# Kernel optimization log

Measured on AMD Instinct MI355X. Metric: run time of the kernel, lower is better.

Reference implementation:

```python
import jax, jax.numpy as jnp
from jax import lax
import numpy as np

H_FEAT = 14
W_FEAT = 14
BN_EPS = 1e-5
NORM_EPS = 1e-12

def _coord_tensor():
    # Python-2 integer division as in the original repo
    c = np.zeros((H_FEAT * W_FEAT, 2), dtype=np.float32)
    for i in range(H_FEAT * W_FEAT):
        c[i, 0] = (i // W_FEAT - H_FEAT // 2) / (H_FEAT / 2.0)
        c[i, 1] = (i % W_FEAT - W_FEAT // 2) / (W_FEAT / 2.0)
    return jnp.asarray(c.reshape(1, H_FEAT, W_FEAT, 2).transpose(0, 3, 1, 2))  # [1,2,14,14]

def _l2norm(x, axis):
    n = jnp.linalg.norm(x, axis=axis, keepdims=True)
    return x / jnp.maximum(n, NORM_EPS)

def _conv2d(x, w, b, pad):
    y = lax.conv_general_dilated(x, w, (1, 1), [(pad, pad), (pad, pad)],
                                 dimension_numbers=("NCHW", "OIHW", "NCHW"))
    return y + b[None, :, None, None]

def _bn_train(x, g, b):
    m = x.mean(axis=(0, 2, 3), keepdims=True)
    v = x.var(axis=(0, 2, 3), keepdims=True)
    return (x - m) * lax.rsqrt(v + BN_EPS) * g[None, :, None, None] + b[None, :, None, None]

def _lstm_scan(emb, Wih, Whh, bih, bhh):
    # emb: [T, B, 300]; PyTorch gate order i,f,g,o
    Hdim = Whh.shape[1]
    B = emb.shape[1]
    def step(carry, x):
        h, c = carry
        gates = x @ Wih.T + h @ Whh.T + bih + bhh  # [B, 4H]
        i, f, g, o = jnp.split(gates, 4, axis=-1)
        c = jax.nn.sigmoid(f) * c + jax.nn.sigmoid(i) * jnp.tanh(g)
        h = jax.nn.sigmoid(o) * jnp.tanh(c)
        return (h, c), h
    init = (jnp.zeros((B, Hdim), emb.dtype), jnp.zeros((B, Hdim), emb.dtype))
    _, hs = lax.scan(step, init, emb)
    return hs  # [T, B, H]

def _resblock(v, coord, c1w, c1b, c2w, c2b, bng, bnb):
    B = v.shape[0]
    vin = jnp.concatenate([v, jnp.broadcast_to(coord, (B, 2, H_FEAT, W_FEAT))], axis=1)
    v1 = jax.nn.relu(_conv2d(vin, c1w, c1b, 0))
    v2 = jax.nn.relu(_bn_train(_conv2d(v1, c2w, c2b, 1), bng, bnb))
    return v2 + v1

def setup_inputs() -> dict:
    key = jax.random.key(0)
    ks = jax.random.split(key, 24)
    B, T, V, E = 128, 45, 10000, 300
    Hh = 1024
    s = 0.02
    inp = {}
    inp["que"] = jax.random.randint(ks[0], (B, T), 0, V, dtype=jnp.int64)
    inp["img"] = jax.random.normal(ks[1], (B, 1024, H_FEAT, W_FEAT), dtype=jnp.float32)
    inp["lookup"] = s * jax.random.normal(ks[2], (V + 1, E), dtype=jnp.float32)
    inp["Wih_f"] = s * jax.random.normal(ks[3], (4 * Hh, E), dtype=jnp.float32)
    inp["Whh_f"] = s * jax.random.normal(ks[4], (4 * Hh, Hh), dtype=jnp.float32)
    inp["bih_f"] = jnp.zeros((4 * Hh,), jnp.float32)
    inp["bhh_f"] = jnp.zeros((4 * Hh,), jnp.float32)
    inp["Wih_b"] = s * jax.random.normal(ks[5], (4 * Hh, E), dtype=jnp.float32)
    inp["Whh_b"] = s * jax.random.normal(ks[6], (4 * Hh, Hh), dtype=jnp.float32)
    inp["bih_b"] = jnp.zeros((4 * Hh,), jnp.float32)
    inp["bhh_b"] = jnp.zeros((4 * Hh,), jnp.float32)
    inp["conv0_w"] = s * jax.random.normal(ks[7], (128, 1026, 3, 3), dtype=jnp.float32)
    inp["conv0_b"] = jnp.zeros((128,), jnp.float32)
    inp["bn0_g"] = jnp.ones((128,), jnp.float32)
    inp["bn0_b"] = jnp.zeros((128,), jnp.float32)
    inp["r1c1_w"] = s * jax.random.normal(ks[8], (128, 130, 1, 1), dtype=jnp.float32)
    inp["r1c1_b"] = jnp.zeros((128,), jnp.float32)
    inp["r1c2_w"] = s * jax.random.normal(ks[9], (128, 128, 3, 3), dtype=jnp.float32)
    inp["r1c2_b"] = jnp.zeros((128,), jnp.float32)
    inp["r1bn_g"] = jnp.ones((128,), jnp.float32)
    inp["r1bn_b"] = jnp.zeros((128,), jnp.float32)
    inp["r2c1_w"] = s * jax.random.normal(ks[10], (128, 130, 1, 1), dtype=jnp.float32)
    inp["r2c1_b"] = jnp.zeros((128,), jnp.float32)
    inp["r2c2_w"] = s * jax.random.normal(ks[11], (128, 128, 3, 3), dtype=jnp.float32)
    inp["r2c2_b"] = jnp.zeros((128,), jnp.float32)
    inp["r2bn_g"] = jnp.ones((128,), jnp.float32)
    inp["r2bn_b"] = jnp.zeros((128,), jnp.float32)
    return inp

def reference(que, img, lookup, Wih_f, Whh_f, bih_f, bhh_f, Wih_b, Whh_b, bih_b, bhh_b,
              conv0_w, conv0_b, bn0_g, bn0_b,
              r1c1_w, r1c1_b, r1c2_w, r1c2_b, r1bn_g, r1bn_b,
              r2c1_w, r2c1_b, r2c2_w, r2c2_b, r2bn_g, r2bn_b):
    coord = _coord_tensor()
    # ---- encoder (LSTM mode) ----
    emb = lookup[que]                      # [B, T, 300]
    emb = jnp.transpose(emb, (1, 0, 2))    # [T, B, 300]
    h_f = _lstm_scan(emb, Wih_f, Whh_f, bih_f, bhh_f)
    h_b = _lstm_scan(emb[::-1], Wih_b, Whh_b, bih_b, bhh_b)[::-1]
    qenc = _l2norm(jnp.concatenate([h_f, h_b], axis=-1), axis=-1)  # [T, B, 2048]
    enc = qenc[-1]                                                  # [B, 2048]
    # ---- image branch ----
    v = _l2norm(img, axis=1)               # per-pixel L2 norm over 1024 channels
    B = v.shape[0]
    v = jnp.concatenate([v, jnp.broadcast_to(coord, (B, 2, H_FEAT, W_FEAT))], axis=1)
    v = jax.nn.relu(_bn_train(_conv2d(v, conv0_w, conv0_b, 1), bn0_g, bn0_b))
    v = _resblock(v, coord, r1c1_w, r1c1_b, r1c2_w, r1c2_b, r1bn_g, r1bn_b)
    v = _resblock(v, coord, r2c1_w, r2c1_b, r2c2_w, r2c2_b, r2bn_g, r2bn_b)
    return (enc, v)
```

## Files before the change

### kernel.cpp

```cpp
#include <hip/hip_runtime.h>
#include <math.h>

#define BB   128
#define T    45
#define E    300
#define HH   1024
#define G4   4096
#define HW   196
#define NPX  (BB*HW)
#define C0   1026
#define CM   128
#define CR   130
#define TCH  15

static __device__ __forceinline__ float sigm(float x) { return 1.f / (1.f + __expf(-x)); }

__global__ void k_embed(const int* __restrict__ que, const float* __restrict__ lookup,
                        float* __restrict__ emb) {
    int idx = blockIdx.x * 256 + threadIdx.x;
    if (idx >= T * BB * E) return;
    int e = idx % E;
    int n = idx / E;
    int b = n % BB;
    int t = n / BB;
    int q = que[b * T + t];
    emb[idx] = lookup[(size_t)q * E + e];
}

template <int BM, int BN, int TM, int TN>
__global__ __launch_bounds__(256) void k_gemm_nt(
    const float* __restrict__ A, int lda,
    const float* __restrict__ Bw, int ldb,
    const float* __restrict__ add,
    const float* __restrict__ bias,
    float* __restrict__ C, int ldc,
    int M, int N, int K, int relu) {
    constexpr int KT = 16;
    constexpr int TX = BN / TN;
    __shared__ float As[KT][BM + 4];
    __shared__ float Bs[KT][BN + 4];
    const int tid = threadIdx.x;
    const int tx = tid % TX, ty = tid / TX;
    const int r0 = blockIdx.x * BM, c0 = blockIdx.y * BN;
    float acc[TM][TN] = {};
    for (int k0 = 0; k0 < K; k0 += KT) {
#pragma unroll
        for (int l = tid; l < BM * KT; l += 256) {
            int m = l / KT, k = l % KT;
            int gm = r0 + m, gk = k0 + k;
            As[k][m] = (gm < M && gk < K) ? A[(size_t)gm * lda + gk] : 0.f;
        }
#pragma unroll
        for (int l = tid; l < BN * KT; l += 256) {
            int n = l / KT, k = l % KT;
            int gn = c0 + n, gk = k0 + k;
            Bs[k][n] = (gn < N && gk < K) ? Bw[(size_t)gn * ldb + gk] : 0.f;
        }
        __syncthreads();
#pragma unroll
        for (int k = 0; k < KT; ++k) {
            float ar[TM], br[TN];
#pragma unroll
            for (int i = 0; i < TM; ++i) ar[i] = As[k][ty * TM + i];
#pragma unroll
            for (int j = 0; j < TN; ++j) br[j] = Bs[k][tx * TN + j];
#pragma unroll
            for (int i = 0; i < TM; ++i)
#pragma unroll
                for (int j = 0; j < TN; ++j) acc[i][j] += ar[i] * br[j];
        }
        __syncthreads();
    }
#pragma unroll
    for (int i = 0; i < TM; ++i) {
        int gm = r0 + ty * TM + i;
        if (gm >= M) continue;
#pragma unroll
        for (int j = 0; j < TN; ++j) {
            int gn = c0 + tx * TN + j;
            if (gn >= N) continue;
            float v = acc[i][j];
            if (add) v += add[(size_t)gm * ldc + gn];
            if (bias) v += bias[gn];
            if (relu) v = fmaxf(v, 0.f);
            C[(size_t)gm * ldc + gn] = v;
        }
    }
}

__global__ void k_pack_wih(const float* __restrict__ Wih, float* __restrict__ o) {
    int idx = blockIdx.x * 256 + threadIdx.x;
    if (idx >= G4 * E) return;
    int k = idx % E;
    int n = idx / E;
    o[idx] = Wih[(size_t)((n & 3) * HH + (n >> 2)) * E + k];
}
__global__ void k_pack_whh(const float* __restrict__ Whh, float* __restrict__ o) {
    int idx = blockIdx.x * 256 + threadIdx.x;
    if (idx >= G4 * HH) return;
    int k = idx & 1023;
    int n = idx >> 10;
    o[idx] = Whh[(size_t)((n & 3) * HH + (n >> 2)) * HH + k];
}
__global__ void k_pack_b4i(const float* __restrict__ bih, const float* __restrict__ bhh,
                           float* __restrict__ out) {
    int n = blockIdx.x * 256 + threadIdx.x;
    if (n >= G4) return;
    int r = (n & 3) * HH + (n >> 2);
    out[n] = bih[r] + bhh[r];
}
__global__ void k_biasadd(const float* __restrict__ bih, const float* __restrict__ bhh,
                          float* __restrict__ out) {
    int idx = blockIdx.x * 256 + threadIdx.x;
    if (idx < G4) out[idx] = bih[idx] + bhh[idx];
}

__global__ void k_cell_plain(float* __restrict__ h, float* __restrict__ c,
                             const float* __restrict__ gx, int first) {
    int idx = blockIdx.x * 256 + threadIdx.x;
    int b = idx >> 10, j = idx & 1023;
    size_t base = (size_t)b * G4 + j;
    float gi = gx[base], gf = gx[base + HH], gg = gx[base + 2 * HH], go = gx[base + 3 * HH];
    float cp = first ? 0.f : c[idx];
    float cn = sigm(gf) * cp + sigm(gi) * tanhf(gg);
    c[idx] = cn;
    h[idx] = sigm(go) * tanhf(cn);
}

__global__ __launch_bounds__(256) void k_lstm_fused(
    const float* __restrict__ h_in, float* __restrict__ c_io,
    const float* __restrict__ gx,
    const float* __restrict__ Wpk,
    float* __restrict__ h_out, int first) {
    __shared__ float As[16][36];
    __shared__ float Bs[16][68];
    const int tid = threadIdx.x;
    const int tx = tid & 15, ty = tid >> 4;
    const int r0 = blockIdx.x * 32;
    const int c0 = blockIdx.y * 64;
    const int ka = tid & 15, ma = tid >> 4;
    float acc[2][4] = {};

#define LSTM_LD(K0)                                                               \
    {                                                                             \
        int gk = (K0) + ka;                                                       \
        rA0 = h_in[(size_t)(r0 + ma) * HH + gk];                                  \
        rA1 = h_in[(size_t)(r0 + ma + 16) * HH + gk];                             \
        const float* wp = Wpk + (size_t)(c0 + ma) * HH + gk;                      \
        rB0 = wp[0];                                                              \
        rB1 = wp[(size_t)16 * HH];                                                \
        rB2 = wp[(size_t)32 * HH];                                                \
        rB3 = wp[(size_t)48 * HH];                                                \
    }

    if (!first) {
        float rA0, rA1, rB0, rB1, rB2, rB3;
        LSTM_LD(0);
        for (int k0 = 0; k0 < HH; k0 += 16) {
            As[ka][ma] = rA0;
            As[ka][ma + 16] = rA1;
            Bs[ka][ma] = rB0;
            Bs[ka][ma + 16] = rB1;
            Bs[ka][ma + 32] = rB2;
            Bs[ka][ma + 48] = rB3;
            __syncthreads();
            if (k0 + 16 < HH) LSTM_LD(k0 + 16);
#pragma unroll
            for (int k = 0; k < 16; ++k) {
                float a0 = As[k][ty * 2], a1 = As[k][ty * 2 + 1];
                float br[4];
#pragma unroll
                for (int j = 0; j < 4; ++j) br[j] = Bs[k][tx * 4 + j];
#pragma unroll
                for (int j = 0; j < 4; ++j) {
                    acc[0][j] += a0 * br[j];
                    acc[1][j] += a1 * br[j];
                }
            }
            __syncthreads();
        }
    }
#undef LSTM_LD
    const int jj4 = c0 + tx * 4;
    const int u = jj4 >> 2;
#pragma unroll
    for (int i = 0; i < 2; ++i) {
        int b = r0 + ty * 2 + i;
        float4 g4 = *(const float4*)&gx[(size_t)b * G4 + jj4];
        float gi = acc[i][0] + g4.x;
        float gf = acc[i][1] + g4.y;
        float gg = acc[i][2] + g4.z;
        float go = acc[i][3] + g4.w;
        size_t ci = (size_t)b * HH + u;
        float cp = first ? 0.f : c_io[ci];
        float cn = sigm(gf) * cp + sigm(gi) * tanhf(gg);
        c_io[ci] = cn;
        h_out[ci] = sigm(go) * tanhf(cn);
    }
}

__global__ void k_enc(const float* __restrict__ hf, const float* __restrict__ hb,
                      float* __restrict__ out) {
    int b = blockIdx.x;
    int tid = threadIdx.x;
    float vals[8];
    float ss = 0.f;
#pragma unroll
    for (int i = 0; i < 8; ++i) {
        int j = i * 256 + tid;
        float v = (j < HH) ? hf[(size_t)b * HH + j] : hb[(size_t)b * HH + (j - HH)];
        vals[i] = v;
        ss += v * v;
    }
    __shared__ float red[256];
    red[tid] = ss;
    __syncthreads();
    for (int s = 128; s > 0; s >>= 1) {
        if (tid < s) red[tid] += red[tid + s];
        __syncthreads();
    }
    float scale = 1.f / fmaxf(sqrtf(red[0]), 1e-12f);
#pragma unroll
    for (int i = 0; i < 8; ++i) out[(size_t)b * 2048 + i * 256 + tid] = vals[i] * scale;
}

__global__ void k_pixssq(const float* __restrict__ img, float* __restrict__ ssq) {
    int b = blockIdx.x >> 4;
    int cc = (blockIdx.x & 15) * 64;
    int p = threadIdx.x;
    if (p >= HW) return;
    const float* base = img + ((size_t)b * 1024 + cc) * HW + p;
    float acc = 0.f;
#pragma unroll 4
    for (int c = 0; c < 64; ++c) {
        float v = base[(size_t)c * HW];
        acc += v * v;
    }
    atomicAdd(&ssq[b * HW + p], acc);
}

__global__ void k_invn(float* __restrict__ ssq) {
    int i = blockIdx.x * 256 + threadIdx.x;
    if (i >= NPX) return;
    ssq[i] = 1.f / fmaxf(sqrtf(ssq[i]), 1e-12f);
}

__global__ void k_packB0(const float* __restrict__ w, float* __restrict__ o) {
    int idx = blockIdx.x * 256 + threadIdx.x;
    if (idx >= 8 * 9 * 1040 * 16) return;
    int oi = idx & 15;
    int r = idx >> 4;
    int c = r % 1040;
    int gt = r / 1040;
    int tap = gt % 9, ocg = gt / 9;
    o[idx] = (c < C0) ? w[((size_t)(ocg * 16 + oi) * C0 + c) * 9 + tap] : 0.f;
}
__global__ void k_packBpm(const float* __restrict__ w, float* __restrict__ o) {
    int idx = blockIdx.x * 256 + threadIdx.x;
    if (idx >= 8 * 9 * 128 * 16) return;
    int oi = idx & 15;
    int r = idx >> 4;
    int c = r % 128;
    int gt = r / 128;
    int tap = gt % 9, ocg = gt / 9;
    o[idx] = w[((size_t)(ocg * 16 + oi) * 128 + c) * 9 + tap];
}

static __device__ __forceinline__ void conv_swz784(int id, int& g, int& ocg, int& z) {
    int s2 = (id & 7) * 98 + (id >> 3);
    g = s2 >> 4;
    int cb = s2 & 15;
    ocg = cb >> 1;
    z = cb & 1;
}

__global__ __launch_bounds__(256) void k_conv0(const float* __restrict__ img,
                                               const float* __restrict__ invn,
                                               const float* __restrict__ wpk,
                                               const float* __restrict__ bias,
                                               float* __restrict__ outParts) {
    __shared__ float As[545][18];
    const int tid = threadIdx.x;
    int g, ocg, z;
    conv_swz784(blockIdx.x, g, ocg, z);
    const int kbeg = z ? 528 : 0;
    const int kend = z ? 1040 : 528;
    float* out = outParts + (size_t)z * NPX * CM;
    const int P0 = g * 512;
    const int gp1 = P0 + tid;
    const int gp2 = gp1 + 256;
    const int p1 = gp1 % HW, p2 = gp2 % HW;
    const int y1 = p1 / 14, x1 = p1 % 14;
    const int y2 = p2 / 14, x2 = p2 % 14;

    const float* sptr[3];
    float sinv[3], scy[3], scx[3];
#pragma unroll
    for (int j = 0; j < 3; ++j) {
        int s = tid + j * 256;
        int gp = P0 - 16 + s;
        bool ok = (s <= 542) && (gp >= 0) && (gp < NPX);
        int gpc = ok ? gp : 0;
        int pp = gpc % HW;
        int bi = gpc / HW;
        sptr[j] = img + ((size_t)bi * 1024) * HW + pp;
        sinv[j] = ok ? invn[gpc] : 0.f;
        scy[j] = ok ? (float)(pp / 14 - 7) * (1.f / 7.f) : 0.f;
        scx[j] = ok ? (float)(pp % 14 - 7) * (1.f / 7.f) : 0.f;
    }

    float acc0[16] = {};
    float acc1[16] = {};
    for (int k0 = kbeg; k0 < kend; k0 += 16) {
        __syncthreads();
        if (k0 < 1024) {
#pragma unroll
            for (int j = 0; j < 3; ++j) {
                int s = tid + j * 256;
                if (j < 2 || s < 545) {
                    const float* pbase = sptr[j] + (size_t)k0 * HW;
                    float inv = sinv[j];
#pragma unroll
                    for (int k = 0; k < 16; ++k) As[s][k] = pbase[(size_t)k * HW] * inv;
                }
            }
        } else {
#pragma unroll
            for (int j = 0; j < 3; ++j) {
                int s = tid + j * 256;
                if (j < 2 || s < 545) {
                    As[s][0] = scy[j];
                    As[s][1] = scx[j];
#pragma unroll
                    for (int k = 2; k < 16; ++k) As[s][k] = 0.f;
                }
            }
        }
        __syncthreads();
        for (int tap = 0; tap < 9; ++tap) {
            const int ky = tap / 3 - 1, kx = tap % 3 - 1;
            const int d = ky * 14 + kx;
            const int of1 = ((unsigned)(y1 + ky) < 14u && (unsigned)(x1 + kx) < 14u)
                                ? (tid + 16 + d) : 544;
            const int of2 = ((unsigned)(y2 + ky) < 14u && (unsigned)(x2 + kx) < 14u)
                                ? (tid + 272 + d) : 544;
            const float4* __restrict__ wq =
                (const float4*)wpk + ((size_t)(ocg * 9 + tap) * 1040 + k0) * 4;
#pragma unroll
            for (int kq = 0; kq < 4; ++kq) {
                float2 a01 = *(const float2*)&As[of1][kq * 4];
                float2 a23 = *(const float2*)&As[of1][kq * 4 + 2];
                float2 b01 = *(const float2*)&As[of2][kq * 4];
                float2 b23 = *(const float2*)&As[of2][kq * 4 + 2];
                float av[4] = {a01.x, a01.y, a23.x, a23.y};
                float bv[4] = {b01.x, b01.y, b23.x, b23.y};
#pragma unroll
                for (int kk = 0; kk < 4; ++kk) {
                    float a = av[kk], b = bv[kk];
                    float4 w0 = wq[0], w1 = wq[1], w2 = wq[2], w3 = wq[3];
                    wq += 4;
                    acc0[0]  += a * w0.x;  acc1[0]  += b * w0.x;
                    acc0[1]  += a * w0.y;  acc1[1]  += b * w0.y;
                    acc0[2]  += a * w0.z;  acc1[2]  += b * w0.z;
                    acc0[3]  += a * w0.w;  acc1[3]  += b * w0.w;
                    acc0[4]  += a * w1.x;  acc1[4]  += b * w1.x;
                    acc0[5]  += a * w1.y;  acc1[5]  += b * w1.y;
                    acc0[6]  += a * w1.z;  acc1[6]  += b * w1.z;
                    acc0[7]  += a * w1.w;  acc1[7]  += b * w1.w;
                    acc0[8]  += a * w2.x;  acc1[8]  += b * w2.x;
                    acc0[9]  += a * w2.y;  acc1[9]  += b * w2.y;
                    acc0[10] += a * w2.z;  acc1[10] += b * w2.z;
                    acc0[11] += a * w2.w;  acc1[11] += b * w2.w;
                    acc0[12] += a * w3.x;  acc1[12] += b * w3.x;
                    acc0[13] += a * w3.y;  acc1[13] += b * w3.y;
                    acc0[14] += a * w3.z;  acc1[14] += b * w3.z;
                    acc0[15] += a * w3.w;  acc1[15] += b * w3.w;
                }
            }
        }
    }
    const float* bp = bias + ocg * 16;
    float* op1 = out + (size_t)gp1 * CM + ocg * 16;
    float* op2 = out + (size_t)gp2 * CM + ocg * 16;
#pragma unroll
    for (int qq = 0; qq < 4; ++qq) {
        float b0 = z ? 0.f : bp[qq * 4 + 0];
        float b1 = z ? 0.f : bp[qq * 4 + 1];
        float b2 = z ? 0.f : bp[qq * 4 + 2];
        float b3 = z ? 0.f : bp[qq * 4 + 3];
        float4 r0, r1;
        r0.x = acc0[qq * 4 + 0] + b0;  r1.x = acc1[qq * 4 + 0] + b0;
        r0.y = acc0[qq * 4 + 1] + b1;  r1.y = acc1[qq * 4 + 1] + b1;
        r0.z = acc0[qq * 4 + 2] + b2;  r1.z = acc1[qq * 4 + 2] + b2;
        r0.w = acc0[qq * 4 + 3] + b3;  r1.w = acc1[qq * 4 + 3] + b3;
        *(float4*)&op1[qq * 4] = r0;
        *(float4*)&op2[qq * 4] = r1;
    }
}

__global__ __launch_bounds__(256) void k_conv_pm(const float* __restrict__ vin,
                                                 const float* __restrict__ wpk,
                                                 const float* __restrict__ bias,
                                                 float* __restrict__ outParts) {
    __shared__ float As[545][18];
    const int tid = threadIdx.x;
    int g, ocg, z;
    conv_swz784(blockIdx.x, g, ocg, z);
    const int kbeg = z * 64;
    float* out = outParts + (size_t)z * NPX * CM;
    const int P0 = g * 512;
    const int gp1 = P0 + tid;
    const int gp2 = gp1 + 256;
    const int p1 = gp1 % HW, p2 = gp2 % HW;
    const int y1 = p1 / 14, x1 = p1 % 14;
    const int y2 = p2 / 14, x2 = p2 % 14;
    float acc0[16] = {};
    float acc1[16] = {};
    for (int k0 = kbeg; k0 < kbeg + 64; k0 += 16) {
        __syncthreads();
        for (int l = tid; l < 545 * 4; l += 256) {
            int s = l >> 2, kq = l & 3;
            int gp = P0 - 16 + s;
            float4 v;
            v.x = v.y = v.z = v.w = 0.f;
            if (s <= 542 && gp >= 0 && gp < NPX)
                v = *(const float4*)&vin[(size_t)gp * CM + k0 + kq * 4];
            As[s][kq * 4 + 0] = v.x;
            As[s][kq * 4 + 1] = v.y;
            As[s][kq * 4 + 2] = v.z;
            As[s][kq * 4 + 3] = v.w;
        }
        __syncthreads();
        for (int tap = 0; tap < 9; ++tap) {
            const int ky = tap / 3 - 1, kx = tap % 3 - 1;
            const int d = ky * 14 + kx;
            const int of1 = ((unsigned)(y1 + ky) < 14u && (unsigned)(x1 + kx) < 14u)
                                ? (tid + 16 + d) : 544;
            const int of2 = ((unsigned)(y2 + ky) < 14u && (unsigned)(x2 + kx) < 14u)
                                ? (tid + 272 + d) : 544;
            const float4* __restrict__ wq =
                (const float4*)wpk + ((size_t)(ocg * 9 + tap) * 128 + k0) * 4;
#pragma unroll
            for (int kq = 0; kq < 4; ++kq) {
                float2 a01 = *(const float2*)&As[of1][kq * 4];
                float2 a23 = *(const float2*)&As[of1][kq * 4 + 2];
                float2 b01 = *(const float2*)&As[of2][kq * 4];
                float2 b23 = *(const float2*)&As[of2][kq * 4 + 2];
                float av[4] = {a01.x, a01.y, a23.x, a23.y};
                float bv[4] = {b01.x, b01.y, b23.x, b23.y};
#pragma unroll
                for (int kk = 0; kk < 4; ++kk) {
                    float a = av[kk], b = bv[kk];
                    float4 w0 = wq[0], w1 = wq[1], w2 = wq[2], w3 = wq[3];
                    wq += 4;
                    acc0[0]  += a * w0.x;  acc1[0]  += b * w0.x;
                    acc0[1]  += a * w0.y;  acc1[1]  += b * w0.y;
                    acc0[2]  += a * w0.z;  acc1[2]  += b * w0.z;
                    acc0[3]  += a * w0.w;  acc1[3]  += b * w0.w;
                    acc0[4]  += a * w1.x;  acc1[4]  += b * w1.x;
                    acc0[5]  += a * w1.y;  acc1[5]  += b * w1.y;
                    acc0[6]  += a * w1.z;  acc1[6]  += b * w1.z;
                    acc0[7]  += a * w1.w;  acc1[7]  += b * w1.w;
                    acc0[8]  += a * w2.x;  acc1[8]  += b * w2.x;
                    acc0[9]  += a * w2.y;  acc1[9]  += b * w2.y;
                    acc0[10] += a * w2.z;  acc1[10] += b * w2.z;
                    acc0[11] += a * w2.w;  acc1[11] += b * w2.w;
                    acc0[12] += a * w3.x;  acc1[12] += b * w3.x;
                    acc0[13] += a * w3.y;  acc1[13] += b * w3.y;
                    acc0[14] += a * w3.z;  acc1[14] += b * w3.z;
                    acc0[15] += a * w3.w;  acc1[15] += b * w3.w;
                }
            }
        }
    }
    const float* bp = bias + ocg * 16;
    float* op1 = out + (size_t)gp1 * CM + ocg * 16;
    float* op2 = out + (size_t)gp2 * CM + ocg * 16;
#pragma unroll
    for (int qq = 0; qq < 4; ++qq) {
        float b0 = z ? 0.f : bp[qq * 4 + 0];
        float b1 = z ? 0.f : bp[qq * 4 + 1];
        float b2 = z ? 0.f : bp[qq * 4 + 2];
        float b3 = z ? 0.f : bp[qq * 4 + 3];
        float4 r0, r1;
        r0.x = acc0[qq * 4 + 0] + b0;  r1.x = acc1[qq * 4 + 0] + b0;
        r0.y = acc0[qq * 4 + 1] + b1;  r1.y = acc1[qq * 4 + 1] + b1;
        r0.z = acc0[qq * 4 + 2] + b2;  r1.z = acc1[qq * 4 + 2] + b2;
        r0.w = acc0[qq * 4 + 3] + b3;  r1.w = acc1[qq * 4 + 3] + b3;
        *(float4*)&op1[qq * 4] = r0;
        *(float4*)&op2[qq * 4] = r1;
    }
}

__global__ void k_bnstats(const float* __restrict__ xa, const float* __restrict__ xb,
                          float* __restrict__ stats) {
    int r0 = blockIdx.x * 224;
    int c = threadIdx.x & 127, rh = threadIdx.x >> 7;
    float s = 0.f, ss = 0.f;
    for (int r = r0 + rh; r < r0 + 224; r += 2) {
        float v = xa[(size_t)r * CM + c] + xb[(size_t)r * CM + c];
        s += v;
        ss += v * v;
    }
    __shared__ float rs[256], rss[256];
    rs[threadIdx.x] = s;
    rss[threadIdx.x] = ss;
    __syncthreads();
    if (threadIdx.x < 128) {
        s = rs[threadIdx.x] + rs[threadIdx.x + 128];
        ss = rss[threadIdx.x] + rss[threadIdx.x + 128];
        atomicAdd(&stats[c], s);
        atomicAdd(&stats[128 + c], ss);
    }
}

__global__ void k_bnfinal(const float* __restrict__ stats, const float* __restrict__ g,
                          const float* __restrict__ b, float* __restrict__ scsh) {
    int c = threadIdx.x;
    if (c >= 128) return;
    float mean = stats[c] / (float)NPX;
    float var = stats[128 + c] / (float)NPX - mean * mean;
    float sc = g[c] * rsqrtf(var + 1e-5f);
    scsh[c] = sc;
    scsh[128 + c] = b[c] - mean * sc;
}

__global__ void k_apply_cat(const float* __restrict__ xa, const float* __restrict__ xb,
                            const float* __restrict__ scsh,
                            const float* __restrict__ addv, float* __restrict__ vinr) {
    int idx = blockIdx.x * 256 + threadIdx.x;
    if (idx >= NPX * CM) return;
    int c = idx & 127;
    int p = idx >> 7;
    float v = fmaxf((xa[idx] + xb[idx]) * scsh[c] + scsh[128 + c], 0.f);
    if (addv) v += addv[idx];
    vinr[(size_t)p * CR + c] = v;
}

__global__ void k_coords_r(float* __restrict__ vinr) {
    int p = blockIdx.x * 256 + threadIdx.x;
    if (p >= NPX) return;
    int pp = p % HW;
    int y = pp / 14, x = pp % 14;
    vinr[(size_t)p * CR + 128] = (float)(y - 7) * (1.f / 7.f);
    vinr[(size_t)p * CR + 129] = (float)(x - 7) * (1.f / 7.f);
}

__global__ void k_final(const float* __restrict__ xa, const float* __restrict__ xb,
                        const float* __restrict__ scsh,
                        const float* __restrict__ addv, float* __restrict__ outv) {
    int idx = blockIdx.x * 256 + threadIdx.x;
    if (idx >= NPX * CM) return;
    int p = idx % HW;
    int o = (idx / HW) & 127;
    int b = idx / (HW * CM);
    size_t pm = ((size_t)b * HW + p) * CM + o;
    outv[idx] = fmaxf((xa[pm] + xb[pm]) * scsh[o] + scsh[128 + o], 0.f) + addv[pm];
}

extern "C" void kernel_launch(void* const* d_in, const int* in_sizes, int n_in,
                              void* d_out, int out_size, void* d_ws, size_t ws_size,
                              hipStream_t stream) {
    const int* que = (const int*)d_in[0];
    const float* img = (const float*)d_in[1];
    const float* lookup = (const float*)d_in[2];
    const float* Wih_f = (const float*)d_in[3];
    const float* Whh_f = (const float*)d_in[4];
    const float* bih_f = (const float*)d_in[5];
    const float* bhh_f = (const float*)d_in[6];
    const float* Wih_b = (const float*)d_in[7];
    const float* bih_b = (const float*)d_in[9];
    const float* bhh_b = (const float*)d_in[10];
    const float* conv0_w = (const float*)d_in[11];
    const float* conv0_b = (const float*)d_in[12];
    const float* bn0_g = (const float*)d_in[13];
    const float* bn0_b = (const float*)d_in[14];
    const float* r1c1_w = (const float*)d_in[15];
    const float* r1c1_b = (const float*)d_in[16];
    const float* r1c2_w = (const float*)d_in[17];
    const float* r1c2_b = (const float*)d_in[18];
    const float* r1bn_g = (const float*)d_in[19];
    const float* r1bn_b = (const float*)d_in[20];
    const float* r2c1_w = (const float*)d_in[21];
    const float* r2c1_b = (const float*)d_in[22];
    const float* r2c2_w = (const float*)d_in[23];
    const float* r2c2_b = (const float*)d_in[24];
    const float* r2bn_g = (const float*)d_in[25];
    const float* r2bn_b = (const float*)d_in[26];
    float* out = (float*)d_out;

    float* ws = (float*)d_ws;
    float* emb = ws;
    float* Xg = emb + 1728000;
    float* WihPk = Xg + 7864320;
    float* WhhPk = WihPk + 1228800;
    float* b4i = WhhPk + 4194304;
    float* b4b = b4i + 4096;
    float* Xb = b4b + 4096;
    float* hA = Xb + 524288;
    float* hB = hA + 131072;
    float* cbuf = hB + 131072;
    float* hbb = cbuf + 131072;
    size_t lstm_end = (size_t)(hbb + 131072 - ws);
    float* invn = ws;
    float* wpk0 = invn + 25088;
    float* wpk1 = wpk0 + 1198080;
    float* wpk2 = wpk1 + 147456;
    float* xa = wpk2 + 147456;
    float* xb = xa + 3211264;
    float* vinr = xb + 3211264;
    float* v1 = vinr + 3261440;
    float* stats = v1 + 3211264;
    float* scsh = stats + 256;
    size_t img_end = (size_t)(scsh + 256 - ws);
    size_t need = (lstm_end > img_end ? lstm_end : img_end) * 4;
    if (ws_size < need) return;

    auto cdiv = [](int a, int b) { return (a + b - 1) / b; };
    const size_t BG = (size_t)BB * G4;

    k_embed<<<cdiv(T * BB * E, 256), 256, 0, stream>>>(que, lookup, emb);
    k_pack_wih<<<cdiv(G4 * E, 256), 256, 0, stream>>>(Wih_f, WihPk);
    k_pack_whh<<<cdiv(G4 * HH, 256), 256, 0, stream>>>(Whh_f, WhhPk);
    k_pack_b4i<<<16, 256, 0, stream>>>(bih_f, bhh_f, b4i);
    k_biasadd<<<16, 256, 0, stream>>>(bih_b, bhh_b, b4b);
    k_gemm_nt<64, 64, 4, 4><<<dim3(2, 64), 256, 0, stream>>>(
        emb + (size_t)(T - 1) * BB * E, E, Wih_b, E, nullptr, b4b, Xb, G4, BB, G4, E, 0);
    k_cell_plain<<<512, 256, 0, stream>>>(hbb, cbuf, Xb, 1);
    float* hp = hA;
    float* hq = hB;
    float* hlast = hA;
    for (int ch = 0; ch < 3; ++ch) {
        int t0 = ch * TCH;
        k_gemm_nt<64, 64, 4, 4><<<dim3(30, 64), 256, 0, stream>>>(
            emb + (size_t)t0 * BB * E, E, WihPk, E, nullptr, b4i, Xg, G4,
            TCH * BB, G4, E, 0);
        for (int s = 0; s < TCH; ++s) {
            int t = t0 + s;
            k_lstm_fused<<<dim3(4, 64), 256, 0, stream>>>(
                hq, cbuf, Xg + (size_t)s * BG, WhhPk, hp, (t == 0) ? 1 : 0);
            hlast = hp;
            float* tmp = hp; hp = hq; hq = tmp;
        }
    }
    k_enc<<<128, 256, 0, stream>>>(hlast, hbb, out);

    hipMemsetAsync(invn, 0, NPX * 4, stream);
    k_pixssq<<<BB * 16, 256, 0, stream>>>(img, invn);
    k_invn<<<cdiv(NPX, 256), 256, 0, stream>>>(invn);
    k_packB0<<<cdiv(8 * 9 * 1040 * 16, 256), 256, 0, stream>>>(conv0_w, wpk0);
    k_packBpm<<<cdiv(8 * 9 * 128 * 16, 256), 256, 0, stream>>>(r1c2_w, wpk1);
    k_packBpm<<<cdiv(8 * 9 * 128 * 16, 256), 256, 0, stream>>>(r2c2_w, wpk2);

    k_conv0<<<784, 256, 0, stream>>>(img, invn, wpk0, conv0_b, xa);
    hipMemsetAsync(stats, 0, 256 * 4, stream);
    k_bnstats<<<112, 256, 0, stream>>>(xa, xb, stats);
    k_bnfinal<<<1, 128, 0, stream>>>(stats, bn0_g, bn0_b, scsh);
    k_apply_cat<<<cdiv(NPX * CM, 256), 256, 0, stream>>>(xa, xb, scsh, nullptr, vinr);
    k_coords_r<<<cdiv(NPX, 256), 256, 0, stream>>>(vinr);

    k_gemm_nt<64, 64, 4, 4><<<dim3(392, 2), 256, 0, stream>>>(
        vinr, CR, r1c1_w, CR, nullptr, r1c1_b, v1, CM, NPX, CM, CR, 1);
    k_conv_pm<<<784, 256, 0, stream>>>(v1, wpk1, r1c2_b, xa);
    hipMemsetAsync(stats, 0, 256 * 4, stream);
    k_bnstats<<<112, 256, 0, stream>>>(xa, xb, stats);
    k_bnfinal<<<1, 128, 0, stream>>>(stats, r1bn_g, r1bn_b, scsh);
    k_apply_cat<<<cdiv(NPX * CM, 256), 256, 0, stream>>>(xa, xb, scsh, v1, vinr);

    k_gemm_nt<64, 64, 4, 4><<<dim3(392, 2), 256, 0, stream>>>(
        vinr, CR, r2c1_w, CR, nullptr, r2c1_b, v1, CM, NPX, CM, CR, 1);
    k_conv_pm<<<784, 256, 0, stream>>>(v1, wpk2, r2c2_b, xa);
    hipMemsetAsync(stats, 0, 256 * 4, stream);
    k_bnstats<<<112, 256, 0, stream>>>(xa, xb, stats);
    k_bnfinal<<<1, 128, 0, stream>>>(stats, r2bn_g, r2bn_b, scsh);
    k_final<<<cdiv(NPX * CM, 256), 256, 0, stream>>>(xa, xb, scsh, v1, out + (size_t)BB * 2048);
}
```

Before: 3.988 ms.

## Halve conv tile size, transpose shared tile to k-major, and shorten K chunks

```diff
diff --git a/kernel.cpp b/kernel.cpp
--- a/kernel.cpp
+++ b/kernel.cpp
@@ -266,29 +266,29 @@
     o[idx] = w[((size_t)(ocg * 16 + oi) * 128 + c) * 9 + tap];
 }
 
-static __device__ __forceinline__ void conv_swz784(int id, int& g, int& ocg, int& z) {
-    int s2 = (id & 7) * 98 + (id >> 3);
+static __device__ __forceinline__ void conv_swz1568(int id, int& g, int& ocg, int& z) {
+    int s2 = (id & 7) * 196 + (id >> 3);
     g = s2 >> 4;
     int cb = s2 & 15;
     ocg = cb >> 1;
     z = cb & 1;
 }
 
-__global__ __launch_bounds__(256) void k_conv0(const float* __restrict__ img,
+__global__ __launch_bounds__(128) void k_conv0(const float* __restrict__ img,
                                                const float* __restrict__ invn,
                                                const float* __restrict__ wpk,
                                                const float* __restrict__ bias,
                                                float* __restrict__ outParts) {
-    __shared__ float As[545][18];
+    __shared__ float As[8][292];
     const int tid = threadIdx.x;
     int g, ocg, z;
-    conv_swz784(blockIdx.x, g, ocg, z);
+    conv_swz1568(blockIdx.x, g, ocg, z);
     const int kbeg = z ? 528 : 0;
-    const int kend = z ? 1040 : 528;
+    const int kend = z ? 1032 : 528;
     float* out = outParts + (size_t)z * NPX * CM;
-    const int P0 = g * 512;
+    const int P0 = g * 256;
     const int gp1 = P0 + tid;
-    const int gp2 = gp1 + 256;
+    const int gp2 = gp1 + 128;
     const int p1 = gp1 % HW, p2 = gp2 % HW;
     const int y1 = p1 / 14, x1 = p1 % 14;
     const int y2 = p2 / 14, x2 = p2 % 14;
@@ -297,9 +297,9 @@
     float sinv[3], scy[3], scx[3];
 #pragma unroll
     for (int j = 0; j < 3; ++j) {
-        int s = tid + j * 256;
+        int s = tid + j * 128;
         int gp = P0 - 16 + s;
-        bool ok = (s <= 542) && (gp >= 0) && (gp < NPX);
+        bool ok = (s < 288) && (gp >= 0) && (gp < NPX);
         int gpc = ok ? gp : 0;
         int pp = gpc % HW;
         int bi = gpc / HW;
@@ -311,28 +311,28 @@
 
     float acc0[16] = {};
     float acc1[16] = {};
-    for (int k0 = kbeg; k0 < kend; k0 += 16) {
+    for (int k0 = kbeg; k0 < kend; k0 += 8) {
         __syncthreads();
-        if (k0 < 1024) {
+        if (k0 != 1024) {
 #pragma unroll
             for (int j = 0; j < 3; ++j) {
-                int s = tid + j * 256;
-                if (j < 2 || s < 545) {
-                    const float* pbase = sptr[j] + (size_t)k0 * HW;
+                int s = tid + j * 128;
+                if (j < 2 || s < 292) {
+                    const float* pb = sptr[j] + (size_t)k0 * HW;
                     float inv = sinv[j];
 #pragma unroll
-                    for (int k = 0; k < 16; ++k) As[s][k] = pbase[(size_t)k * HW] * inv;
+                    for (int k = 0; k < 8; ++k) As[k][s] = pb[(size_t)k * HW] * inv;
                 }
             }
         } else {
 #pragma unroll
             for (int j = 0; j < 3; ++j) {
-                int s = tid + j * 256;
-                if (j < 2 || s < 545) {
-                    As[s][0] = scy[j];
-                    As[s][1] = scx[j];
-#pragma unroll
-                    for (int k = 2; k < 16; ++k) As[s][k] = 0.f;
+                int s = tid + j * 128;
+                if (j < 2 || s < 292) {
+                    As[0][s] = scy[j];
+                    As[1][s] = scx[j];
+#pragma unroll
+                    for (int k = 2; k < 8; ++k) As[k][s] = 0.f;
                 }
             }
         }
@@ -341,41 +341,33 @@
             const int ky = tap / 3 - 1, kx = tap % 3 - 1;
             const int d = ky * 14 + kx;
             const int of1 = ((unsigned)(y1 + ky) < 14u && (unsigned)(x1 + kx) < 14u)
-                                ? (tid + 16 + d) : 544;
+                                ? (tid + 16 + d) : 288;
             const int of2 = ((unsigned)(y2 + ky) < 14u && (unsigned)(x2 + kx) < 14u)
-                                ? (tid + 272 + d) : 544;
+                                ? (tid + 144 + d) : 288;
             const float4* __restrict__ wq =
                 (const float4*)wpk + ((size_t)(ocg * 9 + tap) * 1040 + k0) * 4;
 #pragma unroll
-            for (int kq = 0; kq < 4; ++kq) {
-                float2 a01 = *(const float2*)&As[of1][kq * 4];
-                float2 a23 = *(const float2*)&As[of1][kq * 4 + 2];
-                float2 b01 = *(const float2*)&As[of2][kq * 4];
-                float2 b23 = *(const float2*)&As[of2][kq * 4 + 2];
-                float av[4] = {a01.x, a01.y, a23.x, a23.y};
-                float bv[4] = {b01.x, b01.y, b23.x, b23.y};
-#pragma unroll
-                for (int kk = 0; kk < 4; ++kk) {
-                    float a = av[kk], b = bv[kk];
-                    float4 w0 = wq[0], w1 = wq[1], w2 = wq[2], w3 = wq[3];
-                    wq += 4;
-                    acc0[0]  += a * w0.x;  acc1[0]  += b * w0.x;
-                    acc0[1]  += a * w0.y;  acc1[1]  += b * w0.y;
-                    acc0[2]  += a * w0.z;  acc1[2]  += b * w0.z;
-                    acc0[3]  += a * w0.w;  acc1[3]  += b * w0.w;
-                    acc0[4]  += a * w1.x;  acc1[4]  += b * w1.x;
-                    acc0[5]  += a * w1.y;  acc1[5]  += b * w1.y;
-                    acc0[6]  += a * w1.z;  acc1[6]  += b * w1.z;
-                    acc0[7]  += a * w1.w;  acc1[7]  += b * w1.w;
-                    acc0[8]  += a * w2.x;  acc1[8]  += b * w2.x;
-                    acc0[9]  += a * w2.y;  acc1[9]  += b * w2.y;
-                    acc0[10] += a * w2.z;  acc1[10] += b * w2.z;
-                    acc0[11] += a * w2.w;  acc1[11] += b * w2.w;
-                    acc0[12] += a * w3.x;  acc1[12] += b * w3.x;
-                    acc0[13] += a * w3.y;  acc1[13] += b * w3.y;
-                    acc0[14] += a * w3.z;  acc1[14] += b * w3.z;
-                    acc0[15] += a * w3.w;  acc1[15] += b * w3.w;
-                }
+            for (int k = 0; k < 8; ++k) {
+                float a = As[k][of1];
+                float b = As[k][of2];
+                float4 w0 = wq[0], w1 = wq[1], w2 = wq[2], w3 = wq[3];
+                wq += 4;
+                acc0[0]  += a * w0.x;  acc1[0]  += b * w0.x;
+                acc0[1]  += a * w0.y;  acc1[1]  += b * w0.y;
+                acc0[2]  += a * w0.z;  acc1[2]  += b * w0.z;
+                acc0[3]  += a * w0.w;  acc1[3]  += b * w0.w;
+                acc0[4]  += a * w1.x;  acc1[4]  += b * w1.x;
+                acc0[5]  += a * w1.y;  acc1[5]  += b * w1.y;
+                acc0[6]  += a * w1.z;  acc1[6]  += b * w1.z;
+                acc0[7]  += a * w1.w;  acc1[7]  += b * w1.w;
+                acc0[8]  += a * w2.x;  acc1[8]  += b * w2.x;
+                acc0[9]  += a * w2.y;  acc1[9]  += b * w2.y;
+                acc0[10] += a * w2.z;  acc1[10] += b * w2.z;
+                acc0[11] += a * w2.w;  acc1[11] += b * w2.w;
+                acc0[12] += a * w3.x;  acc1[12] += b * w3.x;
+                acc0[13] += a * w3.y;  acc1[13] += b * w3.y;
+                acc0[14] += a * w3.z;  acc1[14] += b * w3.z;
+                acc0[15] += a * w3.w;  acc1[15] += b * w3.w;
             }
         }
     }
@@ -398,78 +390,87 @@
     }
 }
 
-__global__ __launch_bounds__(256) void k_conv_pm(const float* __restrict__ vin,
+__global__ __launch_bounds__(128) void k_conv_pm(const float* __restrict__ vin,
                                                  const float* __restrict__ wpk,
                                                  const float* __restrict__ bias,
                                                  float* __restrict__ outParts) {
-    __shared__ float As[545][18];
+    __shared__ float As[8][292];
     const int tid = threadIdx.x;
     int g, ocg, z;
-    conv_swz784(blockIdx.x, g, ocg, z);
+    conv_swz1568(blockIdx.x, g, ocg, z);
     const int kbeg = z * 64;
     float* out = outParts + (size_t)z * NPX * CM;
-    const int P0 = g * 512;
+    const int P0 = g * 256;
     const int gp1 = P0 + tid;
-    const int gp2 = gp1 + 256;
+    const int gp2 = gp1 + 128;
     const int p1 = gp1 % HW, p2 = gp2 % HW;
     const int y1 = p1 / 14, x1 = p1 % 14;
     const int y2 = p2 / 14, x2 = p2 % 14;
+
+    const float* sptr[3];
+    float smask[3];
+#pragma unroll
+    for (int j = 0; j < 3; ++j) {
+        int s = tid + j * 128;
+        int gp = P0 - 16 + s;
+        bool ok = (s < 288) && (gp >= 0) && (gp < NPX);
+        sptr[j] = vin + (size_t)(ok ? gp : 0) * CM;
+        smask[j] = ok ? 1.f : 0.f;
+    }
+
     float acc0[16] = {};
     float acc1[16] = {};
-    for (int k0 = kbeg; k0 < kbeg + 64; k0 += 16) {
+    for (int k0 = kbeg; k0 < kbeg + 64; k0 += 8) {
         __syncthreads();
-        for (int l = tid; l < 545 * 4; l += 256) {
-            int s = l >> 2, kq = l & 3;
-            int gp = P0 - 16 + s;
-            float4 v;
-            v.x = v.y = v.z = v.w = 0.f;
-            if (s <= 542 && gp >= 0 && gp < NPX)
-                v = *(const float4*)&vin[(size_t)gp * CM + k0 + kq * 4];
-            As[s][kq * 4 + 0] = v.x;
-            As[s][kq * 4 + 1] = v.y;
-            As[s][kq * 4 + 2] = v.z;
-            As[s][kq * 4 + 3] = v.w;
+#pragma unroll
+        for (int j = 0; j < 3; ++j) {
+            int s = tid + j * 128;
+            if (j < 2 || s < 292) {
+                float4 v0 = *(const float4*)&sptr[j][k0];
+                float4 v1 = *(const float4*)&sptr[j][k0 + 4];
+                float m = smask[j];
+                As[0][s] = v0.x * m;
+                As[1][s] = v0.y * m;
+                As[2][s] = v0.z * m;
+                As[3][s] = v0.w * m;
+                As[4][s] = v1.x * m;
+                As[5][s] = v1.y * m;
+                As[6][s] = v1.z * m;
+                As[7][s] = v1.w * m;
+            }
         }
         __syncthreads();
         for (int tap = 0; tap < 9; ++tap) {
             const int ky = tap / 3 - 1, kx = tap % 3 - 1;
             const int d = ky * 14 + kx;
             const int of1 = ((unsigned)(y1 + ky) < 14u && (unsigned)(x1 + kx) < 14u)
-                                ? (tid + 16 + d) : 544;
+                                ? (tid + 16 + d) : 288;
             const int of2 = ((unsigned)(y2 + ky) < 14u && (unsigned)(x2 + kx) < 14u)
-                                ? (tid + 272 + d) : 544;
+                                ? (tid + 144 + d) : 288;
             const float4* __restrict__ wq =
                 (const float4*)wpk + ((size_t)(ocg * 9 + tap) * 128 + k0) * 4;
 #pragma unroll
-            for (int kq = 0; kq < 4; ++kq) {
-                float2 a01 = *(const float2*)&As[of1][kq * 4];
-                float2 a23 = *(const float2*)&As[of1][kq * 4 + 2];
-                float2 b01 = *(const float2*)&As[of2][kq * 4];
-                float2 b23 = *(const float2*)&As[of2][kq * 4 + 2];
-                float av[4] = {a01.x, a01.y, a23.x, a23.y};
-                float bv[4] = {b01.x, b01.y, b23.x, b23.y};
-#pragma unroll
-                for (int kk = 0; kk < 4; ++kk) {
-                    float a = av[kk], b = bv[kk];
-                    float4 w0 = wq[0], w1 = wq[1], w2 = wq[2], w3 = wq[3];
-                    wq += 4;
-                    acc0[0]  += a * w0.x;  acc1[0]  += b * w0.x;
-                    acc0[1]  += a * w0.y;  acc1[1]  += b * w0.y;
-                    acc0[2]  += a * w0.z;  acc1[2]  += b * w0.z;
-                    acc0[3]  += a * w0.w;  acc1[3]  += b * w0.w;
-                    acc0[4]  += a * w1.x;  acc1[4]  += b * w1.x;
-                    acc0[5]  += a * w1.y;  acc1[5]  += b * w1.y;
-                    acc0[6]  += a * w1.z;  acc1[6]  += b * w1.z;
-                    acc0[7]  += a * w1.w;  acc1[7]  += b * w1.w;
-                    acc0[8]  += a * w2.x;  acc1[8]  += b * w2.x;
-                    acc0[9]  += a * w2.y;  acc1[9]  += b * w2.y;
-                    acc0[10] += a * w2.z;  acc1[10] += b * w2.z;
-                    acc0[11] += a * w2.w;  acc1[11] += b * w2.w;
-                    acc0[12] += a * w3.x;  acc1[12] += b * w3.x;
-                    acc0[13] += a * w3.y;  acc1[13] += b * w3.y;
-                    acc0[14] += a * w3.z;  acc1[14] += b * w3.z;
-                    acc0[15] += a * w3.w;  acc1[15] += b * w3.w;
-                }
+            for (int k = 0; k < 8; ++k) {
+                float a = As[k][of1];
+                float b = As[k][of2];
+                float4 w0 = wq[0], w1 = wq[1], w2 = wq[2], w3 = wq[3];
+                wq += 4;
+                acc0[0]  += a * w0.x;  acc1[0]  += b * w0.x;
+                acc0[1]  += a * w0.y;  acc1[1]  += b * w0.y;
+                acc0[2]  += a * w0.z;  acc1[2]  += b * w0.z;
+                acc0[3]  += a * w0.w;  acc1[3]  += b * w0.w;
+                acc0[4]  += a * w1.x;  acc1[4]  += b * w1.x;
+                acc0[5]  += a * w1.y;  acc1[5]  += b * w1.y;
+                acc0[6]  += a * w1.z;  acc1[6]  += b * w1.z;
+                acc0[7]  += a * w1.w;  acc1[7]  += b * w1.w;
+                acc0[8]  += a * w2.x;  acc1[8]  += b * w2.x;
+                acc0[9]  += a * w2.y;  acc1[9]  += b * w2.y;
+                acc0[10] += a * w2.z;  acc1[10] += b * w2.z;
+                acc0[11] += a * w2.w;  acc1[11] += b * w2.w;
+                acc0[12] += a * w3.x;  acc1[12] += b * w3.x;
+                acc0[13] += a * w3.y;  acc1[13] += b * w3.y;
+                acc0[14] += a * w3.z;  acc1[14] += b * w3.z;
+                acc0[15] += a * w3.w;  acc1[15] += b * w3.w;
             }
         }
     }
@@ -652,7 +653,7 @@
     k_packBpm<<<cdiv(8 * 9 * 128 * 16, 256), 256, 0, stream>>>(r1c2_w, wpk1);
     k_packBpm<<<cdiv(8 * 9 * 128 * 16, 256), 256, 0, stream>>>(r2c2_w, wpk2);
 
-    k_conv0<<<784, 256, 0, stream>>>(img, invn, wpk0, conv0_b, xa);
+    k_conv0<<<1568, 128, 0, stream>>>(img, invn, wpk0, conv0_b, xa);
     hipMemsetAsync(stats, 0, 256 * 4, stream);
     k_bnstats<<<112, 256, 0, stream>>>(xa, xb, stats);
     k_bnfinal<<<1, 128, 0, stream>>>(stats, bn0_g, bn0_b, scsh);
@@ -661,7 +662,7 @@
 
     k_gemm_nt<64, 64, 4, 4><<<dim3(392, 2), 256, 0, stream>>>(
         vinr, CR, r1c1_w, CR, nullptr, r1c1_b, v1, CM, NPX, CM, CR, 1);
-    k_conv_pm<<<784, 256, 0, stream>>>(v1, wpk1, r1c2_b, xa);
+    k_conv_pm<<<1568, 128, 0, stream>>>(v1, wpk1, r1c2_b, xa);
     hipMemsetAsync(stats, 0, 256 * 4, stream);
     k_bnstats<<<112, 256, 0, stream>>>(xa, xb, stats);
     k_bnfinal<<<1, 128, 0, stream>>>(stats, r1bn_g, r1bn_b, scsh);
@@ -669,7 +670,7 @@
 
     k_gemm_nt<64, 64, 4, 4><<<dim3(392, 2), 256, 0, stream>>>(
         vinr, CR, r2c1_w, CR, nullptr, r2c1_b, v1, CM, NPX, CM, CR, 1);
-    k_conv_pm<<<784, 256, 0, stream>>>(v1, wpk2, r2c2_b, xa);
+    k_conv_pm<<<1568, 128, 0, stream>>>(v1, wpk2, r2c2_b, xa);
     hipMemsetAsync(stats, 0, 256 * 4, stream);
     k_bnstats<<<112, 256, 0, stream>>>(xa, xb, stats);
     k_bnfinal<<<1, 128, 0, stream>>>(stats, r2bn_g, r2bn_b, scsh);
```

Result: no change. 3.987 ms (-0.0%).
